# Performance work log

Hardware: AMD Instinct MI355X
Metric: run time of the kernel (lower is better)

The kernel has to match this reference:

```python
import jax, jax.numpy as jnp
import numpy as np

NUM_STEPS = 5
N_NODES = 50000
N_EDGES = 1250000
D_FEAT = 64


def setup_inputs() -> dict:
    key = jax.random.key(0)
    k1, k2, k3, k4 = jax.random.split(key, 4)
    x = jax.random.normal(k1, (N_NODES, D_FEAT), dtype=jnp.float32)
    edge_vals = jax.random.uniform(k2, (N_EDGES,), dtype=jnp.float32)
    edge_rows = jax.random.randint(k3, (N_EDGES,), 0, N_NODES, dtype=jnp.int32)
    edge_cols = jax.random.randint(k4, (N_EDGES,), 0, N_NODES, dtype=jnp.int32)
    return {"x": x, "edge_vals": edge_vals, "edge_rows": edge_rows, "edge_cols": edge_cols}


def reference(x, edge_vals, edge_rows, edge_cols):
    # Repeated SpMM: x <- A @ x, with A given in COO form (rows, cols, vals).
    # torch.sparse.mm(A, x)[i] = sum_{e: rows[e]==i} vals[e] * x[cols[e]]
    n = x.shape[0]

    def spmm(h):
        msgs = edge_vals[:, None] * h[edge_cols]          # [E, D] gather + scale
        return jax.ops.segment_sum(msgs, edge_rows, num_segments=n)  # [N, D] scatter-add

    for _ in range(NUM_STEPS):
        x = spmm(x)
    return x
```

## Files before the change

kernel.cpp:

```cpp
#include <hip/hip_runtime.h>
#include <hip/hip_fp16.h>
#include <stdint.h>

#define D_FEAT 64
#define CH 4096
#define BKT_BITS 8

__global__ __launch_bounds__(256) void bhist_kernel(const int* __restrict__ rows,
                                                    int* __restrict__ block_hist,
                                                    int n_edges, int nb) {
    __shared__ int cnt[256];
    cnt[threadIdx.x] = 0;
    __syncthreads();
    int beg = blockIdx.x * CH;
    int end = min(beg + CH, n_edges);
    for (int i = beg + threadIdx.x; i < end; i += 256)
        atomicAdd(&cnt[rows[i] >> BKT_BITS], 1);
    __syncthreads();
    if (threadIdx.x < nb)
        block_hist[blockIdx.x * nb + threadIdx.x] = cnt[threadIdx.x];
}

__global__ __launch_bounds__(256) void bscan1_kernel(int* __restrict__ block_hist,
                                                     int* __restrict__ btot,
                                                     int nchunks, int nb) {
    __shared__ int buf[256];
    int j = blockIdx.x;
    int t = threadIdx.x;
    int c0 = 2 * t, c1 = 2 * t + 1;
    int v0 = (c0 < nchunks) ? block_hist[(size_t)c0 * nb + j] : 0;
    int v1 = (c1 < nchunks) ? block_hist[(size_t)c1 * nb + j] : 0;
    int loc = v0 + v1;
    buf[t] = loc;
    __syncthreads();
    for (int off = 1; off < 256; off <<= 1) {
        int add = (t >= off) ? buf[t - off] : 0;
        __syncthreads();
        buf[t] += add;
        __syncthreads();
    }
    int excl = buf[t] - loc;
    if (c0 < nchunks) block_hist[(size_t)c0 * nb + j] = excl;
    if (c1 < nchunks) block_hist[(size_t)c1 * nb + j] = excl + v0;
    if (t == 255) btot[j] = buf[255];
}

__global__ __launch_bounds__(256) void bscan2_kernel(const int* __restrict__ btot,
                                                     int* __restrict__ bbase, int nb) {
    __shared__ int buf[256];
    int t = threadIdx.x;
    int v = (t < nb) ? btot[t] : 0;
    buf[t] = v;
    __syncthreads();
    for (int off = 1; off < 256; off <<= 1) {
        int add = (t >= off) ? buf[t - off] : 0;
        __syncthreads();
        buf[t] += add;
        __syncthreads();
    }
    if (t < nb) {
        bbase[t] = buf[t] - v;
        if (t == nb - 1) bbase[nb] = buf[t];
    }
}

__global__ __launch_bounds__(256) void bplace_kernel(const float* __restrict__ vals,
                                                     const int* __restrict__ rows,
                                                     const int* __restrict__ cols,
                                                     const int* __restrict__ block_hist,
                                                     const int* __restrict__ bbase,
                                                     uint2* __restrict__ mid,
                                                     int n_edges, int nb) {
    __shared__ int cnt[256];
    __shared__ int base[256];
    int t = threadIdx.x;
    cnt[t] = 0;
    if (t < nb) base[t] = bbase[t] + block_hist[(size_t)blockIdx.x * nb + t];
    __syncthreads();
    int beg = blockIdx.x * CH;
    int end = min(beg + CH, n_edges);
    for (int i = beg + t; i < end; i += 256) {
        int r = rows[i];
        int b = r >> BKT_BITS;
        int lrank = atomicAdd(&cnt[b], 1);
        __half hv = __float2half_rn(vals[i]);
        unsigned short vb = *reinterpret_cast<unsigned short*>(&hv);
        uint32_t packed = (uint32_t)(cols[i] & 0xFFFF) | ((uint32_t)vb << 16);
        mid[base[b] + lrank] = make_uint2(packed, (uint32_t)r);
    }
}

__global__ __launch_bounds__(256) void bsort_kernel(uint2* __restrict__ mid,
                                                    const int* __restrict__ bbase,
                                                    uint32_t* __restrict__ edges,
                                                    int* __restrict__ offs,
                                                    int n_nodes, int nb) {
    __shared__ int cnt[256];
    __shared__ int buf[256];
    int j = blockIdx.x;
    int t = threadIdx.x;
    int lo = bbase[j];
    int hi = bbase[j + 1];
    cnt[t] = 0;
    __syncthreads();
    const uint32_t RMASK = (1u << BKT_BITS) - 1u;
    for (int i = lo + t; i < hi; i += 256) {
        uint2 e = mid[i];
        int r = (int)(e.y & RMASK);
        int rank = atomicAdd(&cnt[r], 1);
        mid[i].y = e.y | ((uint32_t)rank << 16);
    }
    __syncthreads();
    int v = cnt[t];
    buf[t] = v;
    __syncthreads();
    for (int off = 1; off < 256; off <<= 1) {
        int add = (t >= off) ? buf[t - off] : 0;
        __syncthreads();
        buf[t] += add;
        __syncthreads();
    }
    int start = buf[t] - v;
    int rg = (j << BKT_BITS) + t;
    if (rg <= n_nodes) offs[rg] = lo + start;
    __syncthreads();
    cnt[t] = start;
    __syncthreads();
    for (int i = lo + t; i < hi; i += 256) {
        uint2 e = mid[i];
        int r = (int)(e.y & RMASK);
        int rank = (int)(e.y >> 16);
        edges[lo + cnt[r] + rank] = e.x;
    }
}


__device__ __forceinline__ float unpack_val(uint32_t u) {
    __half_raw hr;
    hr.x = (unsigned short)(u >> 16);
    return __half2float(__half(hr));
}

template <int K, bool IN_F32>
__device__ __forceinline__ void gfma2(const void* __restrict__ hv,
                                      const uint32_t* __restrict__ edges,
                                      int j, int gl, float2& acc) {
    uint32_t u[K];
#pragma unroll
    for (int k = 0; k < K; ++k) u[k] = edges[j + k];
    float2 hh[K];
#pragma unroll
    for (int k = 0; k < K; ++k) {
        size_t c = (size_t)(u[k] & 0xFFFF);
        if (IN_F32) hh[k] = ((const float2*)hv)[c * 32 + gl];
        else        hh[k] = __half22float2(((const __half2*)hv)[c * 32 + gl]);
    }
#pragma unroll
    for (int k = 0; k < K; ++k) {
        float v = unpack_val(u[k]);
        acc.x = fmaf(v, hh[k].x, acc.x);
        acc.y = fmaf(v, hh[k].y, acc.y);
    }
}

template <bool IN_F32, bool OUT_F32>
__global__ __launch_bounds__(256) void spmm2_kernel(const void* __restrict__ hv,
                                                    const uint32_t* __restrict__ edges,
                                                    const int* __restrict__ offs,
                                                    void* __restrict__ outv, int n_nodes) {
    int wave = (int)(((long long)blockIdx.x * blockDim.x + threadIdx.x) >> 6);
    int lane = threadIdx.x & 63;
    int g = lane >> 5;
    int gl = lane & 31;
    int row = wave * 2 + g;
    if (row >= n_nodes) return;
    int beg = offs[row];
    int end = offs[row + 1];
    float2 acc = make_float2(0.f, 0.f);
    int j = beg;
    for (; j + 8 <= end; j += 8) gfma2<8, IN_F32>(hv, edges, j, gl, acc);
    if (j + 4 <= end) { gfma2<4, IN_F32>(hv, edges, j, gl, acc); j += 4; }
    for (; j < end; ++j) {
        uint32_t u = edges[j];
        size_t c = (size_t)(u & 0xFFFF);
        float2 hh = IN_F32 ? ((const float2*)hv)[c * 32 + gl]
                           : __half22float2(((const __half2*)hv)[c * 32 + gl]);
        float v = unpack_val(u);
        acc.x = fmaf(v, hh.x, acc.x);
        acc.y = fmaf(v, hh.y, acc.y);
    }
    if (OUT_F32) {
        ((float2*)outv)[(size_t)row * 32 + gl] = acc;
    } else {
        ((__half2*)outv)[(size_t)row * 32 + gl] = __float22half2_rn(acc);
    }
}


__global__ void spmm_atomic_kernel(const float* __restrict__ h,
                                   const float* __restrict__ vals,
                                   const int* __restrict__ rows,
                                   const int* __restrict__ cols,
                                   float* __restrict__ out,
                                   int n_edges) {
    long long tid = (long long)blockIdx.x * blockDim.x + threadIdx.x;
    int e = (int)(tid >> 6);
    int d = (int)(tid & 63);
    if (e >= n_edges) return;
    float m = vals[e] * h[(size_t)cols[e] * D_FEAT + d];
    atomicAdd(&out[(size_t)rows[e] * D_FEAT + d], m);
}

extern "C" void kernel_launch(void* const* d_in, const int* in_sizes, int n_in,
                              void* d_out, int out_size, void* d_ws, size_t ws_size,
                              hipStream_t stream) {
    const float* x    = (const float*)d_in[0];
    const float* vals = (const float*)d_in[1];
    const int*   rows = (const int*)d_in[2];
    const int*   cols = (const int*)d_in[3];

    int n_nodes = in_sizes[0] / D_FEAT;
    int n_edges = in_sizes[1];

    float* out = (float*)d_out;

    size_t buf_bytes_f32 = (size_t)n_nodes * D_FEAT * sizeof(float);
    size_t buf_bytes_f16 = (size_t)n_nodes * D_FEAT * sizeof(__half);

    auto align_up = [](size_t v) { return (v + 255) & ~(size_t)255; };

    int nb = (n_nodes + 255) >> BKT_BITS;
    int nchunks = (n_edges + CH - 1) / CH;

    size_t pa_b   = align_up(buf_bytes_f16);
    size_t pb_b   = align_up(buf_bytes_f16);
    size_t mid_b  = align_up((size_t)n_edges * sizeof(uint2));
    size_t region1 = pa_b + pb_b;
    if (mid_b > region1) region1 = mid_b;
    size_t edges_b = align_up((size_t)n_edges * sizeof(uint32_t));
    size_t offs_b  = align_up((size_t)(n_nodes + 1) * sizeof(int));
    size_t bh_b    = align_up((size_t)nchunks * nb * sizeof(int));
    size_t bb_b    = align_up((size_t)(nb + 1) * sizeof(int));
    size_t bt_b    = align_up(256 * sizeof(int));
    size_t need = region1 + edges_b + offs_b + bh_b + bb_b + bt_b;

    if (ws_size < need || n_nodes > 65536 || nchunks > 512) {
        float* ws = (float*)d_ws;
        float* dsts[5] = {out, ws, out, ws, out};
        long long total_threads = (long long)n_edges * D_FEAT;
        int block = 256;
        int grid = (int)((total_threads + block - 1) / block);
        const float* src = x;
        for (int s = 0; s < 5; ++s) {
            hipMemsetAsync(dsts[s], 0, buf_bytes_f32, stream);
            spmm_atomic_kernel<<<grid, block, 0, stream>>>(src, vals, rows, cols,
                                                           dsts[s], n_edges);
            src = dsts[s];
        }
        return;
    }

    char* p = (char*)d_ws;
    char* r1 = p;                        p += region1;
    uint32_t* edges      = (uint32_t*)p; p += edges_b;
    int*      offs       = (int*)p;      p += offs_b;
    int*      block_hist = (int*)p;      p += bh_b;
    int*      bbase      = (int*)p;      p += bb_b;
    int*      btot       = (int*)p;      p += bt_b;

    __half* pA = (__half*)r1;
    __half* pB = (__half*)(r1 + pa_b);
    uint2*  mid = (uint2*)r1;

    bhist_kernel<<<nchunks, 256, 0, stream>>>(rows, block_hist, n_edges, nb);
    bscan1_kernel<<<nb, 256, 0, stream>>>(block_hist, btot, nchunks, nb);
    bscan2_kernel<<<1, 256, 0, stream>>>(btot, bbase, nb);
    bplace_kernel<<<nchunks, 256, 0, stream>>>(vals, rows, cols, block_hist, bbase,
                                               mid, n_edges, nb);
    bsort_kernel<<<nb, 256, 0, stream>>>(mid, bbase, edges, offs, n_nodes, nb);

    {
        int rows_per_block = 8;
        int grid = (n_nodes + rows_per_block - 1) / rows_per_block;
        spmm2_kernel<true,  false><<<grid, 256, 0, stream>>>(x,  edges, offs, pA, n_nodes);
        spmm2_kernel<false, false><<<grid, 256, 0, stream>>>(pA, edges, offs, pB, n_nodes);
        spmm2_kernel<false, false><<<grid, 256, 0, stream>>>(pB, edges, offs, pA, n_nodes);
        spmm2_kernel<false, false><<<grid, 256, 0, stream>>>(pA, edges, offs, pB, n_nodes);
        spmm2_kernel<false, true ><<<grid, 256, 0, stream>>>(pB, edges, offs, out, n_nodes);
    }
}
```

Measured before the change: 244.1 us.

## Split feature halves into separate planes and rework bucket sort ranking

Feature vectors are stored as two half-width planes (32 features each), and each SpMM block processes one plane, so the gathered working set per pass halves and may fit better in cache. A new cast kernel converts x to this fp16 split layout up front, replacing the f32-input first pass. The bucket sort now counts first and assigns ranks while scattering, which removes the write-back of ranks into the intermediate buffer. Each edge list is now read twice (once per plane), and the input is rounded to fp16 before the first step instead of being read as f32.

Measured after the change: 238.6 us. 1.02x faster.

```diff
diff --git a/kernel.cpp b/kernel.cpp
--- a/kernel.cpp
+++ b/kernel.cpp
@@ -90,12 +90,13 @@
     }
 }
 
-__global__ __launch_bounds__(256) void bsort_kernel(uint2* __restrict__ mid,
+__global__ __launch_bounds__(256) void bsort_kernel(const uint2* __restrict__ mid,
                                                     const int* __restrict__ bbase,
                                                     uint32_t* __restrict__ edges,
                                                     int* __restrict__ offs,
                                                     int n_nodes, int nb) {
     __shared__ int cnt[256];
+    __shared__ int start[256];
     __shared__ int buf[256];
     int j = blockIdx.x;
     int t = threadIdx.x;
@@ -104,34 +105,44 @@
     cnt[t] = 0;
     __syncthreads();
     const uint32_t RMASK = (1u << BKT_BITS) - 1u;
+    for (int i = lo + t; i < hi; i += 256)
+        atomicAdd(&cnt[mid[i].y & RMASK], 1);
+    __syncthreads();
+    int v = cnt[t];
+    buf[t] = v;
+    __syncthreads();
+    for (int off = 1; off < 256; off <<= 1) {
+        int add = (t >= off) ? buf[t - off] : 0;
+        __syncthreads();
+        buf[t] += add;
+        __syncthreads();
+    }
+    int st = buf[t] - v;
+    start[t] = st;
+    int rg = (j << BKT_BITS) + t;
+    if (rg <= n_nodes) offs[rg] = lo + st;
+    __syncthreads();
+    cnt[t] = 0;
+    __syncthreads();
     for (int i = lo + t; i < hi; i += 256) {
         uint2 e = mid[i];
         int r = (int)(e.y & RMASK);
         int rank = atomicAdd(&cnt[r], 1);
-        mid[i].y = e.y | ((uint32_t)rank << 16);
-    }
-    __syncthreads();
-    int v = cnt[t];
-    buf[t] = v;
-    __syncthreads();
-    for (int off = 1; off < 256; off <<= 1) {
-        int add = (t >= off) ? buf[t - off] : 0;
-        __syncthreads();
-        buf[t] += add;
-        __syncthreads();
-    }
-    int start = buf[t] - v;
-    int rg = (j << BKT_BITS) + t;
-    if (rg <= n_nodes) offs[rg] = lo + start;
-    __syncthreads();
-    cnt[t] = start;
-    __syncthreads();
-    for (int i = lo + t; i < hi; i += 256) {
-        uint2 e = mid[i];
-        int r = (int)(e.y & RMASK);
-        int rank = (int)(e.y >> 16);
-        edges[lo + cnt[r] + rank] = e.x;
-    }
+        edges[lo + start[r] + rank] = e.x;
+    }
+}
+
+__global__ __launch_bounds__(256) void xcast_kernel(const float2* __restrict__ x,
+                                                    __half2* __restrict__ dst, int n_nodes) {
+    int t = blockIdx.x * 256 + threadIdx.x;
+    int total = n_nodes * 32;
+    if (t >= total) return;
+    int node = t >> 5;
+    int k = t & 31;
+    int half = k >> 4;
+    int gl = k & 15;
+    float2 v = x[(size_t)node * 32 + half * 16 + gl];
+    dst[(size_t)half * n_nodes * 16 + (size_t)node * 16 + gl] = __float22half2_rn(v);
 }
 
 
@@ -141,10 +152,10 @@
     return __half2float(__half(hr));
 }
 
-template <int K, bool IN_F32>
-__device__ __forceinline__ void gfma2(const void* __restrict__ hv,
+template <int K>
+__device__ __forceinline__ void gfmaS(const __half2* __restrict__ hv,
                                       const uint32_t* __restrict__ edges,
-                                      int j, int gl, float2& acc) {
+                                      int j, size_t halfbase, int gl, float2& acc) {
     uint32_t u[K];
 #pragma unroll
     for (int k = 0; k < K; ++k) u[k] = edges[j + k];
@@ -152,8 +163,7 @@
 #pragma unroll
     for (int k = 0; k < K; ++k) {
         size_t c = (size_t)(u[k] & 0xFFFF);
-        if (IN_F32) hh[k] = ((const float2*)hv)[c * 32 + gl];
-        else        hh[k] = __half22float2(((const __half2*)hv)[c * 32 + gl]);
+        hh[k] = __half22float2(hv[halfbase + c * 16 + gl]);
     }
 #pragma unroll
     for (int k = 0; k < K; ++k) {
@@ -163,36 +173,41 @@
     }
 }
 
-template <bool IN_F32, bool OUT_F32>
-__global__ __launch_bounds__(256) void spmm2_kernel(const void* __restrict__ hv,
-                                                    const uint32_t* __restrict__ edges,
-                                                    const int* __restrict__ offs,
-                                                    void* __restrict__ outv, int n_nodes) {
-    int wave = (int)(((long long)blockIdx.x * blockDim.x + threadIdx.x) >> 6);
-    int lane = threadIdx.x & 63;
-    int g = lane >> 5;
-    int gl = lane & 31;
-    int row = wave * 2 + g;
+template <bool OUT_F32>
+__global__ __launch_bounds__(256) void spmm_split_kernel(const __half2* __restrict__ hv,
+                                                         const uint32_t* __restrict__ edges,
+                                                         const int* __restrict__ offs,
+                                                         void* __restrict__ outv,
+                                                         int n_nodes, int ntiles) {
+    int bid = blockIdx.x;
+    int half = (bid >> 2) & 1;
+    int tile = (bid >> 3) * 4 + (bid & 3);
+    if (tile >= ntiles) return;
+    int t = threadIdx.x;
+    int warp = t >> 6;
+    int lane = t & 63;
+    int grp = lane >> 4;
+    int gl = lane & 15;
+    int row = tile * 16 + warp * 4 + grp;
     if (row >= n_nodes) return;
+    size_t halfbase = (size_t)half * n_nodes * 16;
     int beg = offs[row];
     int end = offs[row + 1];
     float2 acc = make_float2(0.f, 0.f);
     int j = beg;
-    for (; j + 8 <= end; j += 8) gfma2<8, IN_F32>(hv, edges, j, gl, acc);
-    if (j + 4 <= end) { gfma2<4, IN_F32>(hv, edges, j, gl, acc); j += 4; }
+    for (; j + 8 <= end; j += 8) gfmaS<8>(hv, edges, j, halfbase, gl, acc);
+    if (j + 4 <= end) { gfmaS<4>(hv, edges, j, halfbase, gl, acc); j += 4; }
     for (; j < end; ++j) {
         uint32_t u = edges[j];
-        size_t c = (size_t)(u & 0xFFFF);
-        float2 hh = IN_F32 ? ((const float2*)hv)[c * 32 + gl]
-                           : __half22float2(((const __half2*)hv)[c * 32 + gl]);
+        float2 hh = __half22float2(hv[halfbase + (size_t)(u & 0xFFFF) * 16 + gl]);
         float v = unpack_val(u);
         acc.x = fmaf(v, hh.x, acc.x);
         acc.y = fmaf(v, hh.y, acc.y);
     }
     if (OUT_F32) {
-        ((float2*)outv)[(size_t)row * 32 + gl] = acc;
+        ((float2*)outv)[(size_t)row * 32 + half * 16 + gl] = acc;
     } else {
-        ((__half2*)outv)[(size_t)row * 32 + gl] = __float22half2_rn(acc);
+        ((__half2*)outv)[halfbase + (size_t)row * 16 + gl] = __float22half2_rn(acc);
     }
 }
 
@@ -268,9 +283,9 @@
     int*      bbase      = (int*)p;      p += bb_b;
     int*      btot       = (int*)p;      p += bt_b;
 
-    __half* pA = (__half*)r1;
-    __half* pB = (__half*)(r1 + pa_b);
-    uint2*  mid = (uint2*)r1;
+    __half2* pA = (__half2*)r1;
+    __half2* pB = (__half2*)(r1 + pa_b);
+    uint2*   mid = (uint2*)r1;
 
     bhist_kernel<<<nchunks, 256, 0, stream>>>(rows, block_hist, n_edges, nb);
     bscan1_kernel<<<nb, 256, 0, stream>>>(block_hist, btot, nchunks, nb);
@@ -280,12 +295,15 @@
     bsort_kernel<<<nb, 256, 0, stream>>>(mid, bbase, edges, offs, n_nodes, nb);
 
     {
-        int rows_per_block = 8;
-        int grid = (n_nodes + rows_per_block - 1) / rows_per_block;
-        spmm2_kernel<true,  false><<<grid, 256, 0, stream>>>(x,  edges, offs, pA, n_nodes);
-        spmm2_kernel<false, false><<<grid, 256, 0, stream>>>(pA, edges, offs, pB, n_nodes);
-        spmm2_kernel<false, false><<<grid, 256, 0, stream>>>(pB, edges, offs, pA, n_nodes);
-        spmm2_kernel<false, false><<<grid, 256, 0, stream>>>(pA, edges, offs, pB, n_nodes);
-        spmm2_kernel<false, true ><<<grid, 256, 0, stream>>>(pB, edges, offs, out, n_nodes);
-    }
-}
+        int total = n_nodes * 32;
+        xcast_kernel<<<(total + 255) / 256, 256, 0, stream>>>((const float2*)x, pA, n_nodes);
+
+        int ntiles = (n_nodes + 15) / 16;
+        int grid = ((ntiles + 3) / 4) * 8;
+        spmm_split_kernel<false><<<grid, 256, 0, stream>>>(pA, edges, offs, pB, n_nodes, ntiles);
+        spmm_split_kernel<false><<<grid, 256, 0, stream>>>(pB, edges, offs, pA, n_nodes, ntiles);
+        spmm_split_kernel<false><<<grid, 256, 0, stream>>>(pA, edges, offs, pB, n_nodes, ntiles);
+        spmm_split_kernel<false><<<grid, 256, 0, stream>>>(pB, edges, offs, pA, n_nodes, ntiles);
+        spmm_split_kernel<true ><<<grid, 256, 0, stream>>>(pA, edges, offs, out, n_nodes, ntiles);
+    }
+}
```
